# Kernel optimization log

Hardware: AMD Instinct MI355X
Metric: run time of the kernel (lower is better)

The kernel has to match this reference:

```python
import jax, jax.numpy as jnp
import numpy as np

N_NODES = 50000
N_EDGES = 800000
IN_CH = 256
OUT_CH = 64
HEADS = 4
NEG_SLOPE = 0.2


def setup_inputs() -> dict:
    key = jax.random.key(0)
    k = jax.random.split(key, 7)
    x = jax.random.normal(k[0], (N_NODES, IN_CH), dtype=jnp.float32)
    edge_index = jax.random.randint(k[1], (2, N_EDGES), 0, N_NODES, dtype=jnp.int32)
    # Glorot-style init for the linear projection and attention vectors
    W = jax.random.normal(k[2], (IN_CH, HEADS * OUT_CH), dtype=jnp.float32) / np.sqrt(IN_CH)
    att_src = jax.random.normal(k[3], (HEADS, OUT_CH), dtype=jnp.float32) / np.sqrt(OUT_CH)
    att_dst = jax.random.normal(k[4], (HEADS, OUT_CH), dtype=jnp.float32) / np.sqrt(OUT_CH)
    bias = jnp.zeros((HEADS * OUT_CH,), dtype=jnp.float32)
    return {"x": x, "edge_index": edge_index, "W": W,
            "att_src": att_src, "att_dst": att_dst, "bias": bias}


def reference(x, edge_index, W, att_src, att_dst, bias):
    N = x.shape[0]
    # PyG GATConv default: add self-loops
    loop = jnp.arange(N, dtype=edge_index.dtype)
    src = jnp.concatenate([edge_index[0], loop])
    dst = jnp.concatenate([edge_index[1], loop])

    h = (x @ W).reshape(N, HEADS, OUT_CH)          # [N,H,C]
    a_src = jnp.einsum('nhc,hc->nh', h, att_src)    # [N,H]
    a_dst = jnp.einsum('nhc,hc->nh', h, att_dst)    # [N,H]

    alpha = a_src[src] + a_dst[dst]                 # [E,H]
    alpha = jax.nn.leaky_relu(alpha, NEG_SLOPE)

    # segment softmax over edges grouped by destination node
    amax = jax.ops.segment_max(alpha, dst, num_segments=N)
    amax = jnp.where(jnp.isfinite(amax), amax, 0.0)
    e = jnp.exp(alpha - amax[dst])
    denom = jax.ops.segment_sum(e, dst, num_segments=N)
    coef = e / (denom[dst] + 1e-16)                 # [E,H]

    msg = coef[..., None] * h[src]                  # [E,H,C]
    out = jax.ops.segment_sum(msg, dst, num_segments=N)  # [N,H,C]
    out = out.reshape(N, HEADS * OUT_CH) + bias
    return jax.nn.relu(out)
```

## Files before the change

### kernel.cpp

```cpp
#include <hip/hip_runtime.h>
#include <hip/hip_bf16.h>

#define HC 256
#define NEG_SLOPE 0.2f
#define BM 128
#define BK 64
#define LDK 72

typedef short short8_t __attribute__((ext_vector_type(8)));
typedef float float4_t __attribute__((ext_vector_type(4)));

__device__ __forceinline__ unsigned short f2bf(float f) {
  unsigned u = __float_as_uint(f);
  return (unsigned short)((u + 0x7fffu + ((u >> 16) & 1u)) >> 16);
}
__device__ __forceinline__ float bf2f(unsigned short b) {
  return __uint_as_float(((unsigned)b) << 16);
}

__global__ void wt_kernel(const float* __restrict__ W, unsigned short* __restrict__ Wt)
{
  const int k = blockIdx.x;
  const int n = threadIdx.x;
  Wt[n * 256 + k] = f2bf(W[k * 256 + n]);
}

__global__ __launch_bounds__(256) void gemm_deg(
    const float* __restrict__ x, const unsigned short* __restrict__ Wt,
    const float* __restrict__ att_src, const float* __restrict__ att_dst,
    unsigned short* __restrict__ h, float* __restrict__ a_src,
    float* __restrict__ a_dst, const int* __restrict__ ei,
    int* __restrict__ deg, int E, int nnodes, int degBlocks)
{
  __shared__ unsigned short As[BM * LDK];
  __shared__ unsigned short Bs[256 * LDK];
  const int t = threadIdx.x;

  if (blockIdx.x < degBlocks) {
    const int base = (blockIdx.x * 256 + t) * 4;
    if (base + 3 < E) {
      const int4 d4 = *(const int4*)&ei[E + base];
      atomicAdd(&deg[d4.x], 1);
      atomicAdd(&deg[d4.y], 1);
      atomicAdd(&deg[d4.z], 1);
      atomicAdd(&deg[d4.w], 1);
    } else {
      for (int e = base; e < E; ++e) atomicAdd(&deg[ei[E + e]], 1);
    }
    return;
  }

  const int wv   = t >> 6;
  const int lane = t & 63;
  const int r0   = (blockIdx.x - degBlocks) * BM;

  float4_t acc[8][4] = {};

  for (int k0 = 0; k0 < 256; k0 += BK) {
    __syncthreads();
    {
      const int row = t >> 1, kc = (t & 1) * 32;
      const int gr = r0 + row;
      float4 xv[8];
      if (gr < nnodes) {
        const float4* p = (const float4*)(x + (size_t)gr * 256 + k0 + kc);
        #pragma unroll
        for (int i = 0; i < 8; ++i) xv[i] = p[i];
      } else {
        #pragma unroll
        for (int i = 0; i < 8; ++i) xv[i] = make_float4(0.f, 0.f, 0.f, 0.f);
      }
      const float* f = (const float*)xv;
      unsigned pk[16];
      #pragma unroll
      for (int i = 0; i < 16; ++i) {
        __hip_bfloat162 b2 = __float22bfloat162_rn(make_float2(f[2 * i], f[2 * i + 1]));
        pk[i] = *(unsigned*)&b2;
      }
      uint4* d = (uint4*)&As[row * LDK + kc];
      #pragma unroll
      for (int i = 0; i < 4; ++i)
        d[i] = make_uint4(pk[4 * i], pk[4 * i + 1], pk[4 * i + 2], pk[4 * i + 3]);
    }
    #pragma unroll
    for (int it = 0; it < 4; ++it) {
      const int n = it * 64 + (t >> 2);
      const int kc = (t & 3) * 16;
      const uint4* g = (const uint4*)(Wt + (size_t)n * 256 + k0 + kc);
      uint4 v0 = g[0], v1 = g[1];
      uint4* d = (uint4*)&Bs[n * LDK + kc];
      d[0] = v0; d[1] = v1;
    }
    __syncthreads();

    #pragma unroll
    for (int ks = 0; ks < 2; ++ks) {
      const int ko = ks * 32 + (lane >> 4) * 8;
      short8_t af[8], bfr[4];
      #pragma unroll
      for (int nt = 0; nt < 4; ++nt)
        bfr[nt] = *(const short8_t*)&Bs[(64 * wv + 16 * nt + (lane & 15)) * LDK + ko];
      #pragma unroll
      for (int mt = 0; mt < 8; ++mt)
        af[mt] = *(const short8_t*)&As[(16 * mt + (lane & 15)) * LDK + ko];
      #pragma unroll
      for (int mt = 0; mt < 8; ++mt)
        #pragma unroll
        for (int nt = 0; nt < 4; ++nt)
          acc[mt][nt] = __builtin_amdgcn_mfma_f32_16x16x32_bf16(
              af[mt], bfr[nt], acc[mt][nt], 0, 0, 0);
    }
  }

  const int q = lane >> 4, l15 = lane & 15;
  float atts[4], attd[4];
  #pragma unroll
  for (int nt = 0; nt < 4; ++nt) {
    atts[nt] = att_src[wv * 64 + 16 * nt + l15];
    attd[nt] = att_dst[wv * 64 + 16 * nt + l15];
  }

  #pragma unroll
  for (int mt = 0; mt < 8; ++mt) {
    #pragma unroll
    for (int reg = 0; reg < 4; ++reg) {
      const int row = r0 + 16 * mt + 4 * q + reg;
      const bool ok = row < nnodes;
      float ps = 0.f, pd = 0.f;
      #pragma unroll
      for (int nt = 0; nt < 4; ++nt) {
        const float v = acc[mt][nt][reg];
        if (ok) h[(size_t)row * 256 + 64 * wv + 16 * nt + l15] = f2bf(v);
        ps += v * atts[nt];
        pd += v * attd[nt];
      }
      #pragma unroll
      for (int off = 8; off; off >>= 1) {
        ps += __shfl_down(ps, off, 16);
        pd += __shfl_down(pd, off, 16);
      }
      if (ok && l15 == 0) {
        a_src[row * 4 + wv] = ps;
        a_dst[row * 4 + wv] = pd;
      }
    }
  }
}

__global__ __launch_bounds__(256) void scan_p1(const int* __restrict__ deg,
                                               int* __restrict__ bsum, int n)
{
  __shared__ int ws[4];
  const int t = threadIdx.x, lane = t & 63, wv = t >> 6;
  const int base = blockIdx.x * 1024 + t * 4;
  int4 v = make_int4(0, 0, 0, 0);
  if (base + 3 < n) v = *(const int4*)&deg[base];
  else {
    if (base + 0 < n) v.x = deg[base + 0];
    if (base + 1 < n) v.y = deg[base + 1];
    if (base + 2 < n) v.z = deg[base + 2];
  }
  int s = (v.x + v.y) + (v.z + v.w);
  #pragma unroll
  for (int off = 32; off; off >>= 1) s += __shfl_down(s, off, 64);
  if (lane == 0) ws[wv] = s;
  __syncthreads();
  if (t == 0) bsum[blockIdx.x] = (ws[0] + ws[1]) + (ws[2] + ws[3]);
}

__global__ __launch_bounds__(1024) void scan_p2(const int* __restrict__ bsum,
                                                int* __restrict__ boff,
                                                int* __restrict__ rowptr,
                                                int nb, int n)
{
  __shared__ int wsum[16], woff[16];
  const int t = threadIdx.x, lane = t & 63, wv = t >> 6;
  int v = (t < nb) ? bsum[t] : 0;
  int sc = v;
  #pragma unroll
  for (int off = 1; off < 64; off <<= 1) {
    int u = __shfl_up(sc, off, 64);
    if (lane >= off) sc += u;
  }
  if (lane == 63) wsum[wv] = sc;
  __syncthreads();
  if (t == 0) {
    int run = 0;
    #pragma unroll
    for (int i = 0; i < 16; ++i) { int x = wsum[i]; woff[i] = run; run += x; }
    rowptr[n] = run;
  }
  __syncthreads();
  if (t < nb) boff[t] = woff[wv] + sc - v;
}

__global__ __launch_bounds__(256) void scan_p3(const int* __restrict__ deg,
                                               const int* __restrict__ boff,
                                               int* __restrict__ rowptr,
                                               int* __restrict__ cursor, int n)
{
  __shared__ int wsum[4], woff[4];
  const int t = threadIdx.x, lane = t & 63, wv = t >> 6;
  const int base = blockIdx.x * 1024 + t * 4;
  int4 v = make_int4(0, 0, 0, 0);
  if (base + 3 < n) v = *(const int4*)&deg[base];
  else {
    if (base + 0 < n) v.x = deg[base + 0];
    if (base + 1 < n) v.y = deg[base + 1];
    if (base + 2 < n) v.z = deg[base + 2];
  }
  const int s = (v.x + v.y) + (v.z + v.w);
  int sc = s;
  #pragma unroll
  for (int off = 1; off < 64; off <<= 1) {
    int u = __shfl_up(sc, off, 64);
    if (lane >= off) sc += u;
  }
  if (lane == 63) wsum[wv] = sc;
  __syncthreads();
  if (t == 0) {
    int run = 0;
    #pragma unroll
    for (int i = 0; i < 4; ++i) { int x = wsum[i]; woff[i] = run; run += x; }
  }
  __syncthreads();
  int excl = boff[blockIdx.x] + woff[wv] + (sc - s);
  int4 r;
  r.x = excl;
  r.y = r.x + v.x;
  r.z = r.y + v.y;
  r.w = r.z + v.z;
  if (base + 3 < n) {
    *(int4*)&rowptr[base] = r;
    *(int4*)&cursor[base] = r;
  } else {
    if (base + 0 < n) { rowptr[base + 0] = r.x; cursor[base + 0] = r.x; }
    if (base + 1 < n) { rowptr[base + 1] = r.y; cursor[base + 1] = r.y; }
    if (base + 2 < n) { rowptr[base + 2] = r.z; cursor[base + 2] = r.z; }
  }
}

__device__ __forceinline__ void fill_one(
    int s, int d, int dlo, int dhi, const float* __restrict__ a_src,
    const float* __restrict__ a_dst, int* __restrict__ cursor,
    int* __restrict__ csr_src, float4* __restrict__ wexp)
{
  if (d < dlo || d >= dhi) return;
  const int pos = atomicAdd(&cursor[d], 1);
  csr_src[pos] = s;
  const float4 as = ((const float4*)a_src)[s];
  const float4 ad = ((const float4*)a_dst)[d];
  float4 al;
  al.x = as.x + ad.x; al.y = as.y + ad.y;
  al.z = as.z + ad.z; al.w = as.w + ad.w;
  al.x = al.x > 0.f ? al.x : NEG_SLOPE * al.x;
  al.y = al.y > 0.f ? al.y : NEG_SLOPE * al.y;
  al.z = al.z > 0.f ? al.z : NEG_SLOPE * al.z;
  al.w = al.w > 0.f ? al.w : NEG_SLOPE * al.w;
  al.x = expf(al.x); al.y = expf(al.y); al.z = expf(al.z); al.w = expf(al.w);
  wexp[pos] = al;
}

__global__ __launch_bounds__(256) void fill_csr(
    const int* __restrict__ ei, const float* __restrict__ a_src,
    const float* __restrict__ a_dst, int* __restrict__ cursor,
    int* __restrict__ csr_src, float4* __restrict__ wexp, int E, int nnodes)
{
  const int g    = blockIdx.x & 7;
  const int bg   = blockIdx.x >> 3;
  const int nbg  = gridDim.x >> 3;
  const int gsz  = (nnodes + 7) >> 3;
  const int dlo  = g * gsz;
  const int dhi  = min(dlo + gsz, nnodes);
  const int E4   = E >> 2;

  for (int c = bg * 256 + threadIdx.x; c < E4; c += nbg * 256) {
    const int4 d4 = *(const int4*)&ei[E + 4 * c];
    const int4 s4 = *(const int4*)&ei[4 * c];
    fill_one(s4.x, d4.x, dlo, dhi, a_src, a_dst, cursor, csr_src, wexp);
    fill_one(s4.y, d4.y, dlo, dhi, a_src, a_dst, cursor, csr_src, wexp);
    fill_one(s4.z, d4.z, dlo, dhi, a_src, a_dst, cursor, csr_src, wexp);
    fill_one(s4.w, d4.w, dlo, dhi, a_src, a_dst, cursor, csr_src, wexp);
  }
  for (int e = E4 * 4 + bg * 256 + threadIdx.x; e < E; e += nbg * 256)
    fill_one(ei[e], ei[E + e], dlo, dhi, a_src, a_dst, cursor, csr_src, wexp);
}

__device__ __forceinline__ float4 ld_h(const unsigned short* __restrict__ h,
                                       int row, int cb)
{
  const ushort4 u = *(const ushort4*)&h[(size_t)row * 256 + cb];
  return make_float4(bf2f(u.x), bf2f(u.y), bf2f(u.z), bf2f(u.w));
}

__global__ __launch_bounds__(256) void gather_kernel(
    const int* __restrict__ rowptr, const int* __restrict__ csr_src,
    const float* __restrict__ wexp, const unsigned short* __restrict__ h,
    const float* __restrict__ a_src, const float* __restrict__ a_dst,
    const float* __restrict__ bias, float* __restrict__ out, int n)
{
  const int per8 = gridDim.x >> 3;
  const int vb   = (blockIdx.x & 7) * per8 + (blockIdx.x >> 3);
  const int wave = threadIdx.x >> 6;
  const int lane = threadIdx.x & 63;
  const int d = vb * 4 + wave;
  if (d >= n) return;

  const int head = lane >> 4;
  const int cb   = lane * 4;

  float alpha = a_src[d * 4 + head] + a_dst[d * 4 + head];
  alpha = alpha > 0.f ? alpha : NEG_SLOPE * alpha;
  float w = expf(alpha);
  float dsum = w;
  float4 hv = ld_h(h, d, cb);
  float4 acc = make_float4(w * hv.x, w * hv.y, w * hv.z, w * hv.w);

  int j = rowptr[d];
  const int end = rowptr[d + 1];

  for (; j + 7 < end; j += 8) {
    const int4 sa = *(const int4*)&csr_src[j];
    const int4 sb = *(const int4*)&csr_src[j + 4];
    float wj[8];
    #pragma unroll
    for (int k = 0; k < 8; ++k) wj[k] = wexp[(j + k) * 4 + head];
    const float4 h0 = ld_h(h, sa.x, cb);
    const float4 h1 = ld_h(h, sa.y, cb);
    const float4 h2 = ld_h(h, sa.z, cb);
    const float4 h3 = ld_h(h, sa.w, cb);
    const float4 h4 = ld_h(h, sb.x, cb);
    const float4 h5 = ld_h(h, sb.y, cb);
    const float4 h6 = ld_h(h, sb.z, cb);
    const float4 h7 = ld_h(h, sb.w, cb);
    dsum += ((wj[0] + wj[1]) + (wj[2] + wj[3])) + ((wj[4] + wj[5]) + (wj[6] + wj[7]));
    acc.x += wj[0] * h0.x + wj[1] * h1.x + wj[2] * h2.x + wj[3] * h3.x
           + wj[4] * h4.x + wj[5] * h5.x + wj[6] * h6.x + wj[7] * h7.x;
    acc.y += wj[0] * h0.y + wj[1] * h1.y + wj[2] * h2.y + wj[3] * h3.y
           + wj[4] * h4.y + wj[5] * h5.y + wj[6] * h6.y + wj[7] * h7.y;
    acc.z += wj[0] * h0.z + wj[1] * h1.z + wj[2] * h2.z + wj[3] * h3.z
           + wj[4] * h4.z + wj[5] * h5.z + wj[6] * h6.z + wj[7] * h7.z;
    acc.w += wj[0] * h0.w + wj[1] * h1.w + wj[2] * h2.w + wj[3] * h3.w
           + wj[4] * h4.w + wj[5] * h5.w + wj[6] * h6.w + wj[7] * h7.w;
  }
  for (; j < end; ++j) {
    const int s0 = csr_src[j];
    const float w0 = wexp[j * 4 + head];
    const float4 h0 = ld_h(h, s0, cb);
    dsum += w0;
    acc.x += w0 * h0.x; acc.y += w0 * h0.y;
    acc.z += w0 * h0.z; acc.w += w0 * h0.w;
  }

  const float inv = 1.f / (dsum + 1e-16f);
  const float4 b4 = ((const float4*)bias)[lane];
  float4 o;
  o.x = acc.x * inv + b4.x; o.x = o.x > 0.f ? o.x : 0.f;
  o.y = acc.y * inv + b4.y; o.y = o.y > 0.f ? o.y : 0.f;
  o.z = acc.z * inv + b4.z; o.z = o.z > 0.f ? o.z : 0.f;
  o.w = acc.w * inv + b4.w; o.w = o.w > 0.f ? o.w : 0.f;
  *(float4*)&out[(size_t)d * 256 + cb] = o;
}

extern "C" void kernel_launch(void* const* d_in, const int* in_sizes, int n_in,
                              void* d_out, int out_size, void* d_ws, size_t ws_size,
                              hipStream_t stream)
{
  const float* x       = (const float*)d_in[0];
  const int*   ei      = (const int*)d_in[1];
  const float* W       = (const float*)d_in[2];
  const float* att_src = (const float*)d_in[3];
  const float* att_dst = (const float*)d_in[4];
  const float* bias    = (const float*)d_in[5];

  const int nnodes = in_sizes[0] / HC;
  const int E      = in_sizes[1] / 2;
  const int nb     = (nnodes + 1023) / 1024;
  const int degBlocks  = (E + 1023) / 1024;
  const int gemmBlocks = (nnodes + BM - 1) / BM;
  const int gatherBlocks = (((nnodes + 3) / 4) + 7) & ~7;

  float* out = (float*)d_out;
  char* ws = (char*)d_ws;
  unsigned short* h  = (unsigned short*)ws;
  float* a_src = (float*)(ws + (size_t)nnodes * HC * 2);
  float* a_dst = a_src + (size_t)nnodes * 4;
  unsigned short* Wt = (unsigned short*)(a_dst + (size_t)nnodes * 4);
  int* deg    = (int*)((char*)Wt + 256 * 256 * 2);
  int* rowptr = deg + nnodes;
  int* cursor = rowptr + ((nnodes + 1 + 3) & ~3);
  int* bsum   = cursor + nnodes;
  int* boff   = bsum + ((nb + 3) & ~3);
  float4* wexp = (float4*)(boff + ((nb + 3) & ~3));
  int* csr    = (int*)(wexp + E);

  hipMemsetAsync(deg, 0, (size_t)nnodes * sizeof(int), stream);

  wt_kernel<<<256, 256, 0, stream>>>(W, Wt);

  gemm_deg<<<degBlocks + gemmBlocks, 256, 0, stream>>>(
      x, Wt, att_src, att_dst, h, a_src, a_dst, ei, deg, E, nnodes, degBlocks);

  scan_p1<<<nb, 256, 0, stream>>>(deg, bsum, nnodes);
  scan_p2<<<1, 1024, 0, stream>>>(bsum, boff, rowptr, nb, nnodes);
  scan_p3<<<nb, 256, 0, stream>>>(deg, boff, rowptr, cursor, nnodes);

  fill_csr<<<1024, 256, 0, stream>>>(ei, a_src, a_dst, cursor, csr,
                                     (float4*)wexp, E, nnodes);

  gather_kernel<<<gatherBlocks, 256, 0, stream>>>(
      rowptr, csr, (const float*)wexp, h, a_src, a_dst, bias, out, nnodes);
}
```

Baseline: 294.5 us.

## Restructure GEMM to 64-row tiles reading W from global, move degree count to Wt kernel

The GEMM now stages a whole 64x256 bf16 tile of x in shared memory once, with no k-loop and a single barrier. It reads W fragments directly from global memory (L2/L1 cached) instead of staging them in LDS. The degree-count atomics move from the GEMM launch into the W-transpose kernel, so the GEMM kernel is uniform. Halving the row tile gives more blocks and less LDS per block, which should help occupancy. The cost is uncached-in-LDS global loads for B, which rely on cache hits.

```diff
diff --git a/kernel.cpp b/kernel.cpp
--- a/kernel.cpp
+++ b/kernel.cpp
@@ -3,9 +3,7 @@
 
 #define HC 256
 #define NEG_SLOPE 0.2f
-#define BM 128
-#define BK 64
-#define LDK 72
+#define LDA 264
 
 typedef short short8_t __attribute__((ext_vector_type(8)));
 typedef float float4_t __attribute__((ext_vector_type(4)));
@@ -18,101 +16,86 @@
   return __uint_as_float(((unsigned)b) << 16);
 }
 
-__global__ void wt_kernel(const float* __restrict__ W, unsigned short* __restrict__ Wt)
-{
-  const int k = blockIdx.x;
-  const int n = threadIdx.x;
-  Wt[n * 256 + k] = f2bf(W[k * 256 + n]);
-}
-
-__global__ __launch_bounds__(256) void gemm_deg(
+__global__ void wt_deg(const float* __restrict__ W, unsigned short* __restrict__ Wt,
+                       const int* __restrict__ ei, int* __restrict__ deg, int E)
+{
+  if (blockIdx.x < 256) {
+    const int k = blockIdx.x;
+    const int n = threadIdx.x;
+    Wt[n * 256 + k] = f2bf(W[k * 256 + n]);
+    return;
+  }
+  const int base = ((blockIdx.x - 256) * 256 + threadIdx.x) * 4;
+  if (base + 3 < E) {
+    const int4 d4 = *(const int4*)&ei[E + base];
+    atomicAdd(&deg[d4.x], 1);
+    atomicAdd(&deg[d4.y], 1);
+    atomicAdd(&deg[d4.z], 1);
+    atomicAdd(&deg[d4.w], 1);
+  } else {
+    for (int e = base; e < E; ++e) atomicAdd(&deg[ei[E + e]], 1);
+  }
+}
+
+__global__ __launch_bounds__(256) void gemm_mfma(
     const float* __restrict__ x, const unsigned short* __restrict__ Wt,
     const float* __restrict__ att_src, const float* __restrict__ att_dst,
     unsigned short* __restrict__ h, float* __restrict__ a_src,
-    float* __restrict__ a_dst, const int* __restrict__ ei,
-    int* __restrict__ deg, int E, int nnodes, int degBlocks)
-{
-  __shared__ unsigned short As[BM * LDK];
-  __shared__ unsigned short Bs[256 * LDK];
-  const int t = threadIdx.x;
-
-  if (blockIdx.x < degBlocks) {
-    const int base = (blockIdx.x * 256 + t) * 4;
-    if (base + 3 < E) {
-      const int4 d4 = *(const int4*)&ei[E + base];
-      atomicAdd(&deg[d4.x], 1);
-      atomicAdd(&deg[d4.y], 1);
-      atomicAdd(&deg[d4.z], 1);
-      atomicAdd(&deg[d4.w], 1);
-    } else {
-      for (int e = base; e < E; ++e) atomicAdd(&deg[ei[E + e]], 1);
-    }
-    return;
-  }
-
+    float* __restrict__ a_dst, int nnodes)
+{
+  __shared__ unsigned short As[64 * LDA];
+  const int t    = threadIdx.x;
   const int wv   = t >> 6;
   const int lane = t & 63;
-  const int r0   = (blockIdx.x - degBlocks) * BM;
-
-  float4_t acc[8][4] = {};
-
-  for (int k0 = 0; k0 < 256; k0 += BK) {
-    __syncthreads();
-    {
-      const int row = t >> 1, kc = (t & 1) * 32;
-      const int gr = r0 + row;
-      float4 xv[8];
-      if (gr < nnodes) {
-        const float4* p = (const float4*)(x + (size_t)gr * 256 + k0 + kc);
-        #pragma unroll
-        for (int i = 0; i < 8; ++i) xv[i] = p[i];
-      } else {
-        #pragma unroll
-        for (int i = 0; i < 8; ++i) xv[i] = make_float4(0.f, 0.f, 0.f, 0.f);
+  const int r0   = blockIdx.x * 64;
+
+  {
+    const int row = t >> 2;
+    const int kc  = (t & 3) * 64;
+    const int gr  = r0 + row;
+    unsigned pk[32];
+    if (gr < nnodes) {
+      const float4* p = (const float4*)(x + (size_t)gr * 256 + kc);
+      #pragma unroll
+      for (int i = 0; i < 16; ++i) {
+        const float4 v = p[i];
+        __hip_bfloat162 b0 = __float22bfloat162_rn(make_float2(v.x, v.y));
+        __hip_bfloat162 b1 = __float22bfloat162_rn(make_float2(v.z, v.w));
+        pk[2 * i]     = *(unsigned*)&b0;
+        pk[2 * i + 1] = *(unsigned*)&b1;
       }
-      const float* f = (const float*)xv;
-      unsigned pk[16];
-      #pragma unroll
-      for (int i = 0; i < 16; ++i) {
-        __hip_bfloat162 b2 = __float22bfloat162_rn(make_float2(f[2 * i], f[2 * i + 1]));
-        pk[i] = *(unsigned*)&b2;
-      }
-      uint4* d = (uint4*)&As[row * LDK + kc];
-      #pragma unroll
-      for (int i = 0; i < 4; ++i)
-        d[i] = make_uint4(pk[4 * i], pk[4 * i + 1], pk[4 * i + 2], pk[4 * i + 3]);
+    } else {
+      #pragma unroll
+      for (int i = 0; i < 32; ++i) pk[i] = 0;
     }
-    #pragma unroll
-    for (int it = 0; it < 4; ++it) {
-      const int n = it * 64 + (t >> 2);
-      const int kc = (t & 3) * 16;
-      const uint4* g = (const uint4*)(Wt + (size_t)n * 256 + k0 + kc);
-      uint4 v0 = g[0], v1 = g[1];
-      uint4* d = (uint4*)&Bs[n * LDK + kc];
-      d[0] = v0; d[1] = v1;
-    }
-    __syncthreads();
-
-    #pragma unroll
-    for (int ks = 0; ks < 2; ++ks) {
-      const int ko = ks * 32 + (lane >> 4) * 8;
-      short8_t af[8], bfr[4];
+    uint4* d = (uint4*)&As[row * LDA + kc];
+    #pragma unroll
+    for (int i = 0; i < 8; ++i)
+      d[i] = make_uint4(pk[4 * i], pk[4 * i + 1], pk[4 * i + 2], pk[4 * i + 3]);
+  }
+  __syncthreads();
+
+  const int q = lane >> 4, l15 = lane & 15;
+  float4_t acc[4][4] = {};
+
+  #pragma unroll
+  for (int ks = 0; ks < 8; ++ks) {
+    const int ko = ks * 32 + q * 8;
+    short8_t bfr[4], af[4];
+    #pragma unroll
+    for (int nt = 0; nt < 4; ++nt)
+      bfr[nt] = *(const short8_t*)&Wt[(size_t)(64 * wv + 16 * nt + l15) * 256 + ko];
+    #pragma unroll
+    for (int mt = 0; mt < 4; ++mt)
+      af[mt] = *(const short8_t*)&As[(16 * mt + l15) * LDA + ko];
+    #pragma unroll
+    for (int mt = 0; mt < 4; ++mt)
       #pragma unroll
       for (int nt = 0; nt < 4; ++nt)
-        bfr[nt] = *(const short8_t*)&Bs[(64 * wv + 16 * nt + (lane & 15)) * LDK + ko];
-      #pragma unroll
-      for (int mt = 0; mt < 8; ++mt)
-        af[mt] = *(const short8_t*)&As[(16 * mt + (lane & 15)) * LDK + ko];
-      #pragma unroll
-      for (int mt = 0; mt < 8; ++mt)
-        #pragma unroll
-        for (int nt = 0; nt < 4; ++nt)
-          acc[mt][nt] = __builtin_amdgcn_mfma_f32_16x16x32_bf16(
-              af[mt], bfr[nt], acc[mt][nt], 0, 0, 0);
-    }
-  }
-
-  const int q = lane >> 4, l15 = lane & 15;
+        acc[mt][nt] = __builtin_amdgcn_mfma_f32_16x16x32_bf16(
+            af[mt], bfr[nt], acc[mt][nt], 0, 0, 0);
+  }
+
   float atts[4], attd[4];
   #pragma unroll
   for (int nt = 0; nt < 4; ++nt) {
@@ -121,7 +104,7 @@
   }
 
   #pragma unroll
-  for (int mt = 0; mt < 8; ++mt) {
+  for (int mt = 0; mt < 4; ++mt) {
     #pragma unroll
     for (int reg = 0; reg < 4; ++reg) {
       const int row = r0 + 16 * mt + 4 * q + reg;
@@ -376,8 +359,8 @@
   const int nnodes = in_sizes[0] / HC;
   const int E      = in_sizes[1] / 2;
   const int nb     = (nnodes + 1023) / 1024;
-  const int degBlocks  = (E + 1023) / 1024;
-  const int gemmBlocks = (nnodes + BM - 1) / BM;
+  const int degBlocks    = (E + 1023) / 1024;
+  const int gemmBlocks   = (nnodes + 63) / 64;
   const int gatherBlocks = (((nnodes + 3) / 4) + 7) & ~7;
 
   float* out = (float*)d_out;
@@ -396,10 +379,10 @@
 
   hipMemsetAsync(deg, 0, (size_t)nnodes * sizeof(int), stream);
 
-  wt_kernel<<<256, 256, 0, stream>>>(W, Wt);
-
-  gemm_deg<<<degBlocks + gemmBlocks, 256, 0, stream>>>(
-      x, Wt, att_src, att_dst, h, a_src, a_dst, ei, deg, E, nnodes, degBlocks);
+  wt_deg<<<256 + degBlocks, 256, 0, stream>>>(W, Wt, ei, deg, E);
+
+  gemm_mfma<<<gemmBlocks, 256, 0, stream>>>(
+      x, Wt, att_src, att_dst, h, a_src, a_dst, nnodes);
 
   scan_p1<<<nb, 256, 0, stream>>>(deg, bsum, nnodes);
   scan_p2<<<1, 1024, 0, stream>>>(bsum, boff, rowptr, nb, nnodes);
```

Result: faster. 282.7 us (-4.0%).
